# Kernel optimization log

Hardware: AMD Instinct MI355X
Metric: run time of the kernel (lower is better)

Reference implementation:

```python
import jax, jax.numpy as jnp
import numpy as np

T = 8192   # sequence length (= max_seq_len)
E = 1024   # embedding dim
D = 11     # hard-coded projection dim in source


def setup_inputs() -> dict:
    key = jax.random.key(0)
    ks = jax.random.split(key, 6)
    s_e = 1.0 / np.sqrt(E)
    s_d = 1.0 / np.sqrt(D)
    return {
        "x": jax.random.randint(ks[0], (T,), 0, 32000, dtype=jnp.int64),
        "x_embeddings": jax.random.normal(ks[1], (T, E), dtype=jnp.float32),
        "Wk": jax.random.normal(ks[2], (D, E), dtype=jnp.float32) * s_e,
        "bk": jnp.zeros((D,), dtype=jnp.float32),
        "Wq": jax.random.normal(ks[3], (D, E), dtype=jnp.float32) * s_e,
        "bq": jnp.zeros((D,), dtype=jnp.float32),
        "Wv": jax.random.normal(ks[4], (D, E), dtype=jnp.float32) * s_e,
        "bv": jnp.zeros((D,), dtype=jnp.float32),
        "Wf": jax.random.normal(ks[5], (E, D), dtype=jnp.float32) * s_d,
        "bf": jnp.zeros((E,), dtype=jnp.float32),
    }


def reference(x, x_embeddings, Wk, bk, Wq, bq, Wv, bv, Wf, bf):
    t = x.shape[0]  # static under jit
    k = x_embeddings @ Wk.T + bk            # [T, D]
    q = x_embeddings @ Wq.T + bq            # [T, D]
    v = x_embeddings @ Wv.T + bv            # [T, D]
    att = q @ k.T                           # [T, T]; NOTE: no 1/sqrt(D) scaling in source
    causal = jnp.tril(jnp.ones((t, t), dtype=bool))
    att = jnp.where(causal, att, -jnp.inf)
    att = jax.nn.softmax(att, axis=1)       # dim=1 as in source
    res = att @ v                           # [T, D]
    return res @ Wf.T + bf                  # [T, E]
```

## Files before the change

### kernel.cpp

```cpp
#include <hip/hip_runtime.h>

#define T_SEQ 8192
#define E_DIM 1024
#define QS 36
#define NEC 4
#define ECOLS 256
#define KC 64
#define C2N 32
#define XST 65
#define RB 64
#define JCH 128
#define NJC (T_SEQ / JCH)
#define RPB 512
#define NIB (T_SEQ / RPB)
#define TR 16

__device__ __forceinline__ float2 pkfma(float2 a, float2 b, float2 c) {
    return make_float2(fmaf(a.x, b.x, c.x), fmaf(a.y, b.y, c.y));
}
__device__ __forceinline__ float2 f2(float x, float y) { return make_float2(x, y); }


__global__ __launch_bounds__(256) void prep_wf(const float* __restrict__ Wf,
                                               float* __restrict__ Wfp) {
    int id = blockIdx.x * 256 + threadIdx.x;
    if (id >= E_DIM * 12) return;
    int e = id / 12, d = id % 12;
    Wfp[id] = (d < 11) ? Wf[(size_t)e * 11 + d] : 0.f;
}

__global__ __launch_bounds__(256) void qkv_proj(
    const float* __restrict__ xe,
    const float* __restrict__ Wk, const float* __restrict__ bk,
    const float* __restrict__ Wq, const float* __restrict__ bq,
    const float* __restrict__ Wv, const float* __restrict__ bv,
    float* __restrict__ partQ) {
    const int row0 = blockIdx.x * RB;
    const int ec = blockIdx.y;
    const int lane = threadIdx.x & 63;
    const int wg = __builtin_amdgcn_readfirstlane(threadIdx.x >> 6);

    __shared__ float2 xP[C2N * XST];

    const float* wrow[9]; int col[9]; float bias[9]; bool live[9];
#pragma unroll
    for (int k = 0; k < 9; ++k) {
        int o = wg * 9 + k;
        const float* base; float b = 0.f; int c; bool lv = true;
        if (o < 11)      { base = Wk + (size_t)o * E_DIM;        b = bk[o];      c = o; }
        else if (o < 22) { base = Wq + (size_t)(o - 11) * E_DIM; b = bq[o - 11]; c = o + 1; }
        else if (o < 33) { base = Wv + (size_t)(o - 22) * E_DIM; b = bv[o - 22]; c = o + 2; }
        else             { base = Wk; c = (o == 33) ? 11 : (o == 34) ? 23 : 35; lv = false; }
        wrow[k] = base; col[k] = c; bias[k] = b; live[k] = lv;
    }

    float2 acc[9];
#pragma unroll
    for (int k = 0; k < 9; ++k) acc[k] = f2(0.f, 0.f);

    float4 st[4];
#define STAGE_LOAD(sub)                                                         \
    {                                                                           \
        const int cb = ec * ECOLS + (sub) * KC;                                 \
        _Pragma("unroll")                                                       \
        for (int t = 0; t < 4; ++t) {                                           \
            int idx = threadIdx.x + t * 256;                                    \
            int r = idx >> 4, c4 = idx & 15;                                    \
            st[t] = *(const float4*)(xe + (size_t)(row0 + r) * E_DIM + cb + c4 * 4); \
        }                                                                       \
    }

    STAGE_LOAD(0);
    for (int sub = 0; sub < ECOLS / KC; ++sub) {
        if (sub) __syncthreads();
#pragma unroll
        for (int t = 0; t < 4; ++t) {
            int idx = threadIdx.x + t * 256;
            int r = idx >> 4, c4 = idx & 15;
            float2* d = &xP[(size_t)(c4 * 2) * XST + r];
            d[0]   = f2(st[t].x, st[t].y);
            d[XST] = f2(st[t].z, st[t].w);
        }
        if (sub + 1 < ECOLS / KC) STAGE_LOAD(sub + 1);
        __syncthreads();

        const int cbase = ec * ECOLS + sub * KC;
#pragma unroll 4
        for (int c2 = 0; c2 < C2N; ++c2) {
            float2 xv = xP[c2 * XST + lane];
            const int c = cbase + 2 * c2;
#pragma unroll
            for (int k = 0; k < 9; ++k) {
                const float2 wv = *(const float2*)(wrow[k] + c);
                acc[k] = pkfma(xv, wv, acc[k]);
            }
        }
    }
#undef STAGE_LOAD

    float* dst = partQ + ((size_t)ec * T_SEQ + row0 + lane) * QS;
#pragma unroll
    for (int k = 0; k < 9; ++k) {
        float v = acc[k].x + acc[k].y + (ec == 0 ? bias[k] : 0.f);
        dst[col[k]] = live[k] ? v : 0.f;
    }
}

__global__ __launch_bounds__(256) void reduceQ(const float* __restrict__ partQ,
                                               float* __restrict__ qkvF) {
    const size_t idx = (size_t)blockIdx.x * 256 + threadIdx.x;
    const float4* p = (const float4*)partQ;
    const size_t cs = (size_t)T_SEQ * (QS / 4);
    float4 a = p[idx], b = p[idx + cs], c = p[idx + 2 * cs], d = p[idx + 3 * cs];
    float4 s;
    s.x = (a.x + b.x) + (c.x + d.x);
    s.y = (a.y + b.y) + (c.y + d.y);
    s.z = (a.z + b.z) + (c.z + d.z);
    s.w = (a.w + b.w) + (c.w + d.w);
    ((float4*)qkvF)[idx] = s;
}

#define LOG2E 1.4426950408889634f

template <bool MASK>
__device__ __forceinline__ void attn_body(const float* __restrict__ qkvF,
                                          float* __restrict__ part,
                                          const float* kv, int row0, int j0, int jc) {
    const int r0 = row0 + threadIdx.x * 2;
    const float* qp0 = qkvF + (size_t)r0 * QS + 12;
    const float* qp1 = qp0 + QS;
    float4 qa0 = *(const float4*)(qp0), qa1 = *(const float4*)(qp0 + 4), qa2 = *(const float4*)(qp0 + 8);
    float4 qb0 = *(const float4*)(qp1), qb1 = *(const float4*)(qp1 + 4), qb2 = *(const float4*)(qp1 + 8);
    qa0.x *= LOG2E; qa0.y *= LOG2E; qa0.z *= LOG2E; qa0.w *= LOG2E;
    qa1.x *= LOG2E; qa1.y *= LOG2E; qa1.z *= LOG2E; qa1.w *= LOG2E;
    qa2.x *= LOG2E; qa2.y *= LOG2E; qa2.z *= LOG2E;
    qb0.x *= LOG2E; qb0.y *= LOG2E; qb0.z *= LOG2E; qb0.w *= LOG2E;
    qb1.x *= LOG2E; qb1.y *= LOG2E; qb1.z *= LOG2E; qb1.w *= LOG2E;
    qb2.x *= LOG2E; qb2.y *= LOG2E; qb2.z *= LOG2E;

    float2 a01 = f2(0.f, 0.f), a23 = a01, a45 = a01, a67 = a01, a89 = a01, aXL = a01;
    float2 b01 = a01, b23 = a01, b45 = a01, b67 = a01, b89 = a01, bXL = a01;

    const float* kp = kv;
    float4 cK0 = *(const float4*)(kp),      cK1 = *(const float4*)(kp + 4),  cK2 = *(const float4*)(kp + 8);
    float4 cV0 = *(const float4*)(kp + 24), cV1 = *(const float4*)(kp + 28), cV2 = *(const float4*)(kp + 32);

#pragma unroll 2
    for (int jj = 0; jj < JCH; ++jj) {
        const float* np = kp + ((jj + 1 < JCH) ? QS : 0);
        float4 nK0 = *(const float4*)(np);      float4 nK1 = *(const float4*)(np + 4);
        float4 nK2 = *(const float4*)(np + 8);
        float4 nV0 = *(const float4*)(np + 24); float4 nV1 = *(const float4*)(np + 28);
        float4 nV2 = *(const float4*)(np + 32);

        float2 sa = pkfma(f2(qa0.x, qa0.y), f2(cK0.x, cK0.y),
                    pkfma(f2(qa0.z, qa0.w), f2(cK0.z, cK0.w),
                    pkfma(f2(qa1.x, qa1.y), f2(cK1.x, cK1.y),
                    pkfma(f2(qa1.z, qa1.w), f2(cK1.z, cK1.w),
                    pkfma(f2(qa2.x, qa2.y), f2(cK2.x, cK2.y), f2(0.f, 0.f))))));
        float2 sb = pkfma(f2(qb0.x, qb0.y), f2(cK0.x, cK0.y),
                    pkfma(f2(qb0.z, qb0.w), f2(cK0.z, cK0.w),
                    pkfma(f2(qb1.x, qb1.y), f2(cK1.x, cK1.y),
                    pkfma(f2(qb1.z, qb1.w), f2(cK1.z, cK1.w),
                    pkfma(f2(qb2.x, qb2.y), f2(cK2.x, cK2.y), f2(0.f, 0.f))))));
        float pa = exp2f(sa.x + sa.y + qa2.z * cK2.z);
        float pb = exp2f(sb.x + sb.y + qb2.z * cK2.z);
        if (MASK) {
            pa = (j0 + jj <= r0)     ? pa : 0.f;
            pb = (j0 + jj <= r0 + 1) ? pb : 0.f;
        }
        float2 pa2 = f2(pa, pa), pb2 = f2(pb, pb);
        a01 = pkfma(pa2, f2(cV0.x, cV0.y), a01);
        a23 = pkfma(pa2, f2(cV0.z, cV0.w), a23);
        a45 = pkfma(pa2, f2(cV1.x, cV1.y), a45);
        a67 = pkfma(pa2, f2(cV1.z, cV1.w), a67);
        a89 = pkfma(pa2, f2(cV2.x, cV2.y), a89);
        aXL = pkfma(pa2, f2(cV2.z, 1.f),   aXL);
        b01 = pkfma(pb2, f2(cV0.x, cV0.y), b01);
        b23 = pkfma(pb2, f2(cV0.z, cV0.w), b23);
        b45 = pkfma(pb2, f2(cV1.x, cV1.y), b45);
        b67 = pkfma(pb2, f2(cV1.z, cV1.w), b67);
        b89 = pkfma(pb2, f2(cV2.x, cV2.y), b89);
        bXL = pkfma(pb2, f2(cV2.z, 1.f),   bXL);
        cK0 = nK0; cK1 = nK1; cK2 = nK2; cV0 = nV0; cV1 = nV1; cV2 = nV2;
        kp += QS;
    }

    float* dst = part + ((size_t)jc * T_SEQ + r0) * 12;
    float4 t;
    t.x = a01.x; t.y = a01.y; t.z = a23.x; t.w = a23.y; *(float4*)(dst + 0)  = t;
    t.x = a45.x; t.y = a45.y; t.z = a67.x; t.w = a67.y; *(float4*)(dst + 4)  = t;
    t.x = a89.x; t.y = a89.y; t.z = aXL.x; t.w = aXL.y; *(float4*)(dst + 8)  = t;
    t.x = b01.x; t.y = b01.y; t.z = b23.x; t.w = b23.y; *(float4*)(dst + 12) = t;
    t.x = b45.x; t.y = b45.y; t.z = b67.x; t.w = b67.y; *(float4*)(dst + 16) = t;
    t.x = b89.x; t.y = b89.y; t.z = bXL.x; t.w = bXL.y; *(float4*)(dst + 20) = t;
}

__global__ __launch_bounds__(256, 4) void attn(const float* __restrict__ qkvF,
                                               float* __restrict__ part) {
    const int ib = blockIdx.x, jc = blockIdx.y;
    if (jc > 4 * ib + 3) return;
    const int row0 = ib * RPB, j0 = jc * JCH;

    __shared__ float kv[JCH * QS];
    {
        const float4* src = (const float4*)(qkvF + (size_t)j0 * QS);
        float4* dst = (float4*)kv;
        for (int idx = threadIdx.x; idx < JCH * (QS / 4); idx += 256)
            dst[idx] = src[idx];
    }
    __syncthreads();

    if (jc < 4 * ib)
        attn_body<false>(qkvF, part, kv, row0, j0, jc);
    else
        attn_body<true>(qkvF, part, kv, row0, j0, jc);
}

__global__ __launch_bounds__(256) void pass2(const float* __restrict__ part,
                                             const float* __restrict__ Wfp,
                                             const float* __restrict__ bf,
                                             float* __restrict__ out) {
    const int t0 = blockIdx.x * TR;
    __shared__ float res[TR][12];
    const int cnt = t0 / JCH + 1;
    if (threadIdx.x < TR * 12) {
        const float* p = part + (size_t)t0 * 12 + threadIdx.x;
        const size_t S = (size_t)T_SEQ * 12;
        float v0 = 0.f, v1 = 0.f, v2 = 0.f, v3 = 0.f;
        int c = 0;
        for (; c + 4 <= cnt; c += 4) {
            v0 += p[(size_t)c * S];       v1 += p[(size_t)(c + 1) * S];
            v2 += p[(size_t)(c + 2) * S]; v3 += p[(size_t)(c + 3) * S];
        }
        for (; c < cnt; ++c) v0 += p[(size_t)c * S];
        float v = (v0 + v1) + (v2 + v3);
        const int d = threadIdx.x % 12;
        res[threadIdx.x / 12][d] = (d == 11) ? (1.f / v) : v;
    }
    __syncthreads();

    const int e0 = threadIdx.x * 4;
    float4 wf[4][3];
#pragma unroll
    for (int ee = 0; ee < 4; ++ee) {
        const float4* wp = (const float4*)(Wfp + (size_t)(e0 + ee) * 12);
        wf[ee][0] = wp[0]; wf[ee][1] = wp[1]; wf[ee][2] = wp[2];
    }
    const float4 bv = *(const float4*)(bf + e0);

    for (int r = 0; r < TR; ++r) {
        float rr[12];
#pragma unroll
        for (int d = 0; d < 12; ++d) rr[d] = res[r][d];
        float2 a0 = f2(0.f, 0.f), a1 = a0, a2 = a0, a3 = a0;
#pragma unroll
        for (int d = 0; d < 10; d += 2) {
            float2 rv = f2(rr[d], rr[d + 1]);
            a0 = pkfma(rv, f2(((const float*)&wf[0][0])[d], ((const float*)&wf[0][0])[d + 1]), a0);
            a1 = pkfma(rv, f2(((const float*)&wf[1][0])[d], ((const float*)&wf[1][0])[d + 1]), a1);
            a2 = pkfma(rv, f2(((const float*)&wf[2][0])[d], ((const float*)&wf[2][0])[d + 1]), a2);
            a3 = pkfma(rv, f2(((const float*)&wf[3][0])[d], ((const float*)&wf[3][0])[d + 1]), a3);
        }
        const float rl = rr[11];
        float4 ov;
        ov.x = (a0.x + a0.y + rr[10] * wf[0][2].z) * rl + bv.x;
        ov.y = (a1.x + a1.y + rr[10] * wf[1][2].z) * rl + bv.y;
        ov.z = (a2.x + a2.y + rr[10] * wf[2][2].z) * rl + bv.z;
        ov.w = (a3.x + a3.y + rr[10] * wf[3][2].z) * rl + bv.w;
        *(float4*)(out + (size_t)(t0 + r) * E_DIM + e0) = ov;
    }
}

extern "C" void kernel_launch(void* const* d_in, const int* in_sizes, int n_in,
                              void* d_out, int out_size, void* d_ws, size_t ws_size,
                              hipStream_t stream) {
    const float* xe = (const float*)d_in[1];
    const float* Wk = (const float*)d_in[2];
    const float* bk = (const float*)d_in[3];
    const float* Wq = (const float*)d_in[4];
    const float* bq = (const float*)d_in[5];
    const float* Wv = (const float*)d_in[6];
    const float* bv = (const float*)d_in[7];
    const float* Wf = (const float*)d_in[8];
    const float* bf = (const float*)d_in[9];
    float* out = (float*)d_out;

    float* partQ = (float*)d_ws;
    float* qkvF  = partQ + (size_t)NEC * T_SEQ * QS;
    float* part  = qkvF + (size_t)T_SEQ * QS;
    float* wfp   = part + (size_t)NJC * T_SEQ * 12;

    prep_wf<<<(E_DIM * 12 + 255) / 256, 256, 0, stream>>>(Wf, wfp);
    qkv_proj<<<dim3(T_SEQ / RB, NEC), 256, 0, stream>>>(xe, Wk, bk, Wq, bq, Wv, bv, partQ);
    reduceQ<<<(T_SEQ * (QS / 4)) / 256, 256, 0, stream>>>(partQ, qkvF);
    attn<<<dim3(NIB, NJC), 256, 0, stream>>>(qkvF, part);
    pass2<<<T_SEQ / TR, 256, 0, stream>>>(part, wfp, bf, out);
}
```

Measured before the change: 193.3 us.

## Rebalance causal attention with paired key chunks and compact K/V staging

The attention grid now uses 64-key chunks and fixed 64 slots. Each block handles chunk jc and, when it is still causal, chunk jc+64, which evens out work across blocks and shrinks the partial buffer. K and V are repacked into a 24-float shared-memory stride, and the mask is applied on every iteration instead of through a templated unmasked path. The projection split doubles to 8 column groups, and the workspace is reorganised so the partial-projection buffer is reused for attention partials. The always-on mask adds per-iteration selects, and the extra staging adds a second barrier round.

Measured after the change: 193.0 us. Within noise of the previous version (-0.2%).

```diff
diff --git a/kernel.cpp b/kernel.cpp
--- a/kernel.cpp
+++ b/kernel.cpp
@@ -3,17 +3,19 @@
 #define T_SEQ 8192
 #define E_DIM 1024
 #define QS 36
-#define NEC 4
-#define ECOLS 256
+#define NEC 8
+#define ECOLS 128
 #define KC 64
 #define C2N 32
 #define XST 65
 #define RB 64
-#define JCH 128
-#define NJC (T_SEQ / JCH)
+#define JCH 64
+#define NSLOT 64
 #define RPB 512
 #define NIB (T_SEQ / RPB)
+#define KVW 24
 #define TR 16
+#define LOG2E 1.4426950408889634f
 
 __device__ __forceinline__ float2 pkfma(float2 a, float2 b, float2 c) {
     return make_float2(fmaf(a.x, b.x, c.x), fmaf(a.y, b.y, c.y));
@@ -111,22 +113,78 @@
     const size_t idx = (size_t)blockIdx.x * 256 + threadIdx.x;
     const float4* p = (const float4*)partQ;
     const size_t cs = (size_t)T_SEQ * (QS / 4);
-    float4 a = p[idx], b = p[idx + cs], c = p[idx + 2 * cs], d = p[idx + 3 * cs];
-    float4 s;
-    s.x = (a.x + b.x) + (c.x + d.x);
-    s.y = (a.y + b.y) + (c.y + d.y);
-    s.z = (a.z + b.z) + (c.z + d.z);
-    s.w = (a.w + b.w) + (c.w + d.w);
+    float4 s = make_float4(0.f, 0.f, 0.f, 0.f);
+#pragma unroll
+    for (int c = 0; c < NEC; ++c) {
+        float4 a = p[idx + (size_t)c * cs];
+        s.x += a.x; s.y += a.y; s.z += a.z; s.w += a.w;
+    }
     ((float4*)qkvF)[idx] = s;
 }
 
-#define LOG2E 1.4426950408889634f
-
-template <bool MASK>
-__device__ __forceinline__ void attn_body(const float* __restrict__ qkvF,
-                                          float* __restrict__ part,
-                                          const float* kv, int row0, int j0, int jc) {
+__device__ __forceinline__ void attn_chunk(const float* kv, int j0, int r0,
+    const float4& qa0, const float4& qa1, const float4& qa2,
+    const float4& qb0, const float4& qb1, const float4& qb2,
+    float2& a01, float2& a23, float2& a45, float2& a67, float2& a89, float2& aXL,
+    float2& b01, float2& b23, float2& b45, float2& b67, float2& b89, float2& bXL) {
+#pragma unroll 2
+    for (int jj = 0; jj < JCH; ++jj) {
+        const float* kp = kv + jj * KVW;
+        const float4 kA = *(const float4*)(kp);
+        const float4 kB = *(const float4*)(kp + 4);
+        const float4 kC = *(const float4*)(kp + 8);
+        const float4 vA = *(const float4*)(kp + 12);
+        const float4 vB = *(const float4*)(kp + 16);
+        const float4 vC = *(const float4*)(kp + 20);
+
+        float2 sa = pkfma(f2(qa0.x, qa0.y), f2(kA.x, kA.y),
+                    pkfma(f2(qa0.z, qa0.w), f2(kA.z, kA.w),
+                    pkfma(f2(qa1.x, qa1.y), f2(kB.x, kB.y),
+                    pkfma(f2(qa1.z, qa1.w), f2(kB.z, kB.w),
+                    pkfma(f2(qa2.x, qa2.y), f2(kC.x, kC.y), f2(0.f, 0.f))))));
+        float2 sb = pkfma(f2(qb0.x, qb0.y), f2(kA.x, kA.y),
+                    pkfma(f2(qb0.z, qb0.w), f2(kA.z, kA.w),
+                    pkfma(f2(qb1.x, qb1.y), f2(kB.x, kB.y),
+                    pkfma(f2(qb1.z, qb1.w), f2(kB.z, kB.w),
+                    pkfma(f2(qb2.x, qb2.y), f2(kC.x, kC.y), f2(0.f, 0.f))))));
+        float pa = exp2f(sa.x + sa.y + qa2.z * kC.z);
+        float pb = exp2f(sb.x + sb.y + qb2.z * kC.z);
+        const int j = j0 + jj;
+        pa = (j <= r0)     ? pa : 0.f;
+        pb = (j <= r0 + 1) ? pb : 0.f;
+        float2 pa2 = f2(pa, pa), pb2 = f2(pb, pb);
+        a01 = pkfma(pa2, f2(vA.x, vA.y), a01);
+        a23 = pkfma(pa2, f2(vA.z, vA.w), a23);
+        a45 = pkfma(pa2, f2(vB.x, vB.y), a45);
+        a67 = pkfma(pa2, f2(vB.z, vB.w), a67);
+        a89 = pkfma(pa2, f2(vC.x, vC.y), a89);
+        aXL = pkfma(pa2, f2(vC.z, 1.f),  aXL);
+        b01 = pkfma(pb2, f2(vA.x, vA.y), b01);
+        b23 = pkfma(pb2, f2(vA.z, vA.w), b23);
+        b45 = pkfma(pb2, f2(vB.x, vB.y), b45);
+        b67 = pkfma(pb2, f2(vB.z, vB.w), b67);
+        b89 = pkfma(pb2, f2(vC.x, vC.y), b89);
+        bXL = pkfma(pb2, f2(vC.z, 1.f),  bXL);
+    }
+}
+
+__device__ __forceinline__ void stage_kv(const float* __restrict__ qkvF,
+                                         float* kv, int j0) {
+    for (int idx = threadIdx.x; idx < JCH * 6; idx += 256) {
+        int row = idx / 6, f = idx % 6;
+        int srcOff = f * 4 + (f >= 3 ? 12 : 0);
+        float4 v = *(const float4*)(qkvF + (size_t)(j0 + row) * QS + srcOff);
+        *(float4*)(kv + row * KVW + f * 4) = v;
+    }
+}
+
+__global__ __launch_bounds__(256, 4) void attn(const float* __restrict__ qkvF,
+                                               float* __restrict__ part) {
+    const int ib = blockIdx.x, jc = blockIdx.y;
+    if (jc > 8 * ib + 7) return;
+    const int row0 = ib * RPB;
     const int r0 = row0 + threadIdx.x * 2;
+
     const float* qp0 = qkvF + (size_t)r0 * QS + 12;
     const float* qp1 = qp0 + QS;
     float4 qa0 = *(const float4*)(qp0), qa1 = *(const float4*)(qp0 + 4), qa2 = *(const float4*)(qp0 + 8);
@@ -141,49 +199,21 @@
     float2 a01 = f2(0.f, 0.f), a23 = a01, a45 = a01, a67 = a01, a89 = a01, aXL = a01;
     float2 b01 = a01, b23 = a01, b45 = a01, b67 = a01, b89 = a01, bXL = a01;
 
-    const float* kp = kv;
-    float4 cK0 = *(const float4*)(kp),      cK1 = *(const float4*)(kp + 4),  cK2 = *(const float4*)(kp + 8);
-    float4 cV0 = *(const float4*)(kp + 24), cV1 = *(const float4*)(kp + 28), cV2 = *(const float4*)(kp + 32);
-
-#pragma unroll 2
-    for (int jj = 0; jj < JCH; ++jj) {
-        const float* np = kp + ((jj + 1 < JCH) ? QS : 0);
-        float4 nK0 = *(const float4*)(np);      float4 nK1 = *(const float4*)(np + 4);
-        float4 nK2 = *(const float4*)(np + 8);
-        float4 nV0 = *(const float4*)(np + 24); float4 nV1 = *(const float4*)(np + 28);
-        float4 nV2 = *(const float4*)(np + 32);
-
-        float2 sa = pkfma(f2(qa0.x, qa0.y), f2(cK0.x, cK0.y),
-                    pkfma(f2(qa0.z, qa0.w), f2(cK0.z, cK0.w),
-                    pkfma(f2(qa1.x, qa1.y), f2(cK1.x, cK1.y),
-                    pkfma(f2(qa1.z, qa1.w), f2(cK1.z, cK1.w),
-                    pkfma(f2(qa2.x, qa2.y), f2(cK2.x, cK2.y), f2(0.f, 0.f))))));
-        float2 sb = pkfma(f2(qb0.x, qb0.y), f2(cK0.x, cK0.y),
-                    pkfma(f2(qb0.z, qb0.w), f2(cK0.z, cK0.w),
-                    pkfma(f2(qb1.x, qb1.y), f2(cK1.x, cK1.y),
-                    pkfma(f2(qb1.z, qb1.w), f2(cK1.z, cK1.w),
-                    pkfma(f2(qb2.x, qb2.y), f2(cK2.x, cK2.y), f2(0.f, 0.f))))));
-        float pa = exp2f(sa.x + sa.y + qa2.z * cK2.z);
-        float pb = exp2f(sb.x + sb.y + qb2.z * cK2.z);
-        if (MASK) {
-            pa = (j0 + jj <= r0)     ? pa : 0.f;
-            pb = (j0 + jj <= r0 + 1) ? pb : 0.f;
-        }
-        float2 pa2 = f2(pa, pa), pb2 = f2(pb, pb);
-        a01 = pkfma(pa2, f2(cV0.x, cV0.y), a01);
-        a23 = pkfma(pa2, f2(cV0.z, cV0.w), a23);
-        a45 = pkfma(pa2, f2(cV1.x, cV1.y), a45);
-        a67 = pkfma(pa2, f2(cV1.z, cV1.w), a67);
-        a89 = pkfma(pa2, f2(cV2.x, cV2.y), a89);
-        aXL = pkfma(pa2, f2(cV2.z, 1.f),   aXL);
-        b01 = pkfma(pb2, f2(cV0.x, cV0.y), b01);
-        b23 = pkfma(pb2, f2(cV0.z, cV0.w), b23);
-        b45 = pkfma(pb2, f2(cV1.x, cV1.y), b45);
-        b67 = pkfma(pb2, f2(cV1.z, cV1.w), b67);
-        b89 = pkfma(pb2, f2(cV2.x, cV2.y), b89);
-        bXL = pkfma(pb2, f2(cV2.z, 1.f),   bXL);
-        cK0 = nK0; cK1 = nK1; cK2 = nK2; cV0 = nV0; cV1 = nV1; cV2 = nV2;
-        kp += QS;
+    __shared__ float kv[JCH * KVW];
+
+    const int j0A = jc * JCH;
+    stage_kv(qkvF, kv, j0A);
+    __syncthreads();
+    attn_chunk(kv, j0A, r0, qa0, qa1, qa2, qb0, qb1, qb2,
+               a01, a23, a45, a67, a89, aXL, b01, b23, b45, b67, b89, bXL);
+
+    const int j0B = (jc + NSLOT) * JCH;
+    if (j0B <= row0 + RPB - 1) {
+        __syncthreads();
+        stage_kv(qkvF, kv, j0B);
+        __syncthreads();
+        attn_chunk(kv, j0B, r0, qa0, qa1, qa2, qb0, qb1, qb2,
+                   a01, a23, a45, a67, a89, aXL, b01, b23, b45, b67, b89, bXL);
     }
 
     float* dst = part + ((size_t)jc * T_SEQ + r0) * 12;
@@ -196,47 +226,29 @@
     t.x = b89.x; t.y = b89.y; t.z = bXL.x; t.w = bXL.y; *(float4*)(dst + 20) = t;
 }
 
-__global__ __launch_bounds__(256, 4) void attn(const float* __restrict__ qkvF,
-                                               float* __restrict__ part) {
-    const int ib = blockIdx.x, jc = blockIdx.y;
-    if (jc > 4 * ib + 3) return;
-    const int row0 = ib * RPB, j0 = jc * JCH;
-
-    __shared__ float kv[JCH * QS];
-    {
-        const float4* src = (const float4*)(qkvF + (size_t)j0 * QS);
-        float4* dst = (float4*)kv;
-        for (int idx = threadIdx.x; idx < JCH * (QS / 4); idx += 256)
-            dst[idx] = src[idx];
-    }
-    __syncthreads();
-
-    if (jc < 4 * ib)
-        attn_body<false>(qkvF, part, kv, row0, j0, jc);
-    else
-        attn_body<true>(qkvF, part, kv, row0, j0, jc);
-}
-
 __global__ __launch_bounds__(256) void pass2(const float* __restrict__ part,
                                              const float* __restrict__ Wfp,
                                              const float* __restrict__ bf,
                                              float* __restrict__ out) {
     const int t0 = blockIdx.x * TR;
     __shared__ float res[TR][12];
-    const int cnt = t0 / JCH + 1;
+    int cnt = t0 / JCH + 1;
+    if (cnt > NSLOT) cnt = NSLOT;
     if (threadIdx.x < TR * 12) {
         const float* p = part + (size_t)t0 * 12 + threadIdx.x;
         const size_t S = (size_t)T_SEQ * 12;
-        float v0 = 0.f, v1 = 0.f, v2 = 0.f, v3 = 0.f;
+        float v[8];
+#pragma unroll
+        for (int u = 0; u < 8; ++u) v[u] = 0.f;
         int c = 0;
-        for (; c + 4 <= cnt; c += 4) {
-            v0 += p[(size_t)c * S];       v1 += p[(size_t)(c + 1) * S];
-            v2 += p[(size_t)(c + 2) * S]; v3 += p[(size_t)(c + 3) * S];
+        for (; c + 8 <= cnt; c += 8) {
+#pragma unroll
+            for (int u = 0; u < 8; ++u) v[u] += p[(size_t)(c + u) * S];
         }
-        for (; c < cnt; ++c) v0 += p[(size_t)c * S];
-        float v = (v0 + v1) + (v2 + v3);
+        for (; c < cnt; ++c) v[0] += p[(size_t)c * S];
+        float s = ((v[0] + v[1]) + (v[2] + v[3])) + ((v[4] + v[5]) + (v[6] + v[7]));
         const int d = threadIdx.x % 12;
-        res[threadIdx.x / 12][d] = (d == 11) ? (1.f / v) : v;
+        res[threadIdx.x / 12][d] = (d == 11) ? (1.f / s) : s;
     }
     __syncthreads();
 
@@ -286,14 +298,14 @@
     const float* bf = (const float*)d_in[9];
     float* out = (float*)d_out;
 
-    float* partQ = (float*)d_ws;
-    float* qkvF  = partQ + (size_t)NEC * T_SEQ * QS;
-    float* part  = qkvF + (size_t)T_SEQ * QS;
-    float* wfp   = part + (size_t)NJC * T_SEQ * 12;
+    float* qkvF  = (float*)d_ws;
+    float* wfp   = qkvF + (size_t)T_SEQ * QS;
+    float* partQ = wfp + (size_t)E_DIM * 12;
+    float* part  = partQ;
 
     prep_wf<<<(E_DIM * 12 + 255) / 256, 256, 0, stream>>>(Wf, wfp);
     qkv_proj<<<dim3(T_SEQ / RB, NEC), 256, 0, stream>>>(xe, Wk, bk, Wq, bq, Wv, bv, partQ);
     reduceQ<<<(T_SEQ * (QS / 4)) / 256, 256, 0, stream>>>(partQ, qkvF);
-    attn<<<dim3(NIB, NJC), 256, 0, stream>>>(qkvF, part);
+    attn<<<dim3(NIB, NSLOT), 256, 0, stream>>>(qkvF, part);
     pass2<<<T_SEQ / TR, 256, 0, stream>>>(part, wfp, bf, out);
 }
```
